# Optimization experiments

Hardware: AMD Instinct MI355X
Metric: run time of the kernel (lower is better)

## Reference

```python
import jax, jax.numpy as jnp
import numpy as np

A_BIT = 4
W_BIT = 4
IN_PLANES = 32
OUT_PLANES = 32
EXPANSION = 6
PLANES = EXPANSION * IN_PLANES  # 192


def _fake_quant(x, bits):
    """Per-tensor symmetric fake quantization to `bits` (round + clip, dequantized)."""
    qmax = 2.0 ** (bits - 1) - 1.0
    scale = jnp.maximum(jnp.max(jnp.abs(x)) / qmax, 1e-8)
    y = x / scale
    # straight-through round
    yq = jnp.clip(y + jax.lax.stop_gradient(jnp.round(y) - y), -qmax - 1.0, qmax)
    return yq * scale


def _conv(x, w, stride=1, padding=0, groups=1):
    return jax.lax.conv_general_dilated(
        x, w,
        window_strides=(stride, stride),
        padding=[(padding, padding), (padding, padding)],
        dimension_numbers=("NCHW", "OIHW", "NCHW"),
        feature_group_count=groups,
    )


def _qconv(x, w, stride=1, padding=0, groups=1):
    # FuseConv2dQ: fake-quantize activation (a_bit) and weight (w_bit), then fp conv
    return _conv(_fake_quant(x, A_BIT), _fake_quant(w, W_BIT),
                 stride=stride, padding=padding, groups=groups)


def setup_inputs() -> dict:
    key = jax.random.key(0)
    k0, k1, k2, k3 = jax.random.split(key, 4)
    x = jax.random.normal(k0, (32, IN_PLANES, 112, 112), dtype=jnp.float32)
    # conv1: 1x1 expand  [planes, in_planes, 1, 1]
    w1 = jax.random.normal(k1, (PLANES, IN_PLANES, 1, 1), dtype=jnp.float32) * 0.1
    # conv2: 3x3 depthwise, groups=planes -> [planes, 1, 3, 3]
    w2 = jax.random.normal(k2, (PLANES, 1, 3, 3), dtype=jnp.float32) * 0.1
    # conv3: 1x1 project  [out_planes, planes, 1, 1]
    w3 = jax.random.normal(k3, (OUT_PLANES, PLANES, 1, 1), dtype=jnp.float32) * 0.1
    return {"x": x, "w1": w1, "w2": w2, "w3": w3}


def reference(x, w1, w2, w3):
    out = jax.nn.relu(_qconv(x, w1))                                   # expand 1x1
    out = jax.nn.relu(_qconv(out, w2, stride=1, padding=1, groups=PLANES))  # depthwise 3x3
    out = _qconv(out, w3)                                              # project 1x1
    # stride == 1 and in_planes == out_planes -> identity shortcut
    return out + x
```

## Files before the change

### kernel.cpp

```cpp
#include <hip/hip_runtime.h>

#define NB   32
#define CIN  32
#define PL   192
#define CP   96
#define NG1  4
#define NG3  24
#define HH   112
#define WID  112
#define HW   12544
#define COUT 32
#define SEGS 784
#define SEGROW 7
#define PXB  1568
#define SEG8 14
#define RT8  784

#define W2POFF 64
#define W1NOFF (W2POFF + PL*4)
#define W3NOFF (W1NOFF + NG1*PL)
#define Q1OFF_BYTES 65536
#define QBYTES ((size_t)NB*CP*HW)

__device__ __forceinline__ int sdot4(unsigned int a, unsigned int b, int c) {
#if defined(__has_builtin) && __has_builtin(__builtin_amdgcn_sdot4)
  return __builtin_amdgcn_sdot4((int)a, (int)b, c, false);
#else
#pragma unroll
  for (int i = 0; i < 4; ++i)
    c += ((int)(a << (24 - 8 * i)) >> 24) * ((int)(b << (24 - 8 * i)) >> 24);
  return c;
#endif
}

__device__ __forceinline__ int sdot8(unsigned int a, unsigned int b, int c) {
#if defined(__has_builtin) && __has_builtin(__builtin_amdgcn_sdot8)
  return __builtin_amdgcn_sdot8((int)a, (int)b, c, false);
#else
#pragma unroll
  for (int i = 0; i < 8; ++i)
    c += ((int)(a << (28 - 4 * i)) >> 28) * ((int)(b << (28 - 4 * i)) >> 28);
  return c;
#endif
}

template <int SH>
__device__ __forceinline__ unsigned int winsh(unsigned int hi, unsigned int lo) {
#if defined(__has_builtin) && __has_builtin(__builtin_amdgcn_perm)
  const unsigned int sel = (SH == 1) ? 0x04030201u : (SH == 2) ? 0x05040302u : 0x06050403u;
  return __builtin_amdgcn_perm(hi, lo, sel);
#else
  return (lo >> (8 * SH)) | (hi << (32 - 8 * SH));
#endif
}

__device__ __forceinline__ float quant87(float v, float s) {
  return fminf(fmaxf(rintf(v / s), -8.0f), 7.0f);
}

__device__ __forceinline__ void block_max_commit(int lmax, int* __restrict__ slot) {
  __shared__ int red[4];
  for (int o = 32; o; o >>= 1) lmax = max(lmax, __shfl_down(lmax, o));
  if ((threadIdx.x & 63) == 0) red[threadIdx.x >> 6] = lmax;
  __syncthreads();
  if (threadIdx.x == 0) {
    int m = max(max(red[0], red[1]), max(red[2], red[3]));
    int cur = *(const volatile int*)slot;
    if (m > cur) atomicMax(slot, m);
  }
}

__global__ void kzero(int* __restrict__ wsi) {
  if (threadIdx.x < 16) wsi[threadIdx.x] = 0;
}

__global__ void kmax_x(const float* __restrict__ x, int n4, int* __restrict__ slot) {
  const float4* x4 = (const float4*)x;
  float m = 0.f;
  for (int i = blockIdx.x * blockDim.x + threadIdx.x; i < n4; i += gridDim.x * blockDim.x) {
    float4 v = x4[i];
    m = fmaxf(fmaxf(fabsf(v.x), fabsf(v.y)), fmaxf(fmaxf(fabsf(v.z), fabsf(v.w)), m));
  }
  block_max_commit(__float_as_int(m), slot);
}

__global__ void kmax_w(const float* __restrict__ w1, const float* __restrict__ w2,
                       const float* __restrict__ w3, int* __restrict__ slots) {
  const float* p; int n;
  if (blockIdx.x == 0)      { p = w1; n = PL * CIN; }
  else if (blockIdx.x == 1) { p = w2; n = PL * 9; }
  else                      { p = w3; n = COUT * PL; }
  float m = 0.f;
  for (int i = threadIdx.x; i < n; i += blockDim.x) m = fmaxf(m, fabsf(p[i]));
  for (int o = 32; o; o >>= 1) m = fmaxf(m, __shfl_down(m, o));
  if ((threadIdx.x & 63) == 0) atomicMax(slots + 1 + blockIdx.x, __float_as_int(m));
}

__global__ void kprep(const float* __restrict__ w1, const float* __restrict__ w2,
                      const float* __restrict__ w3, float* __restrict__ wsf) {
  int* wsi = (int*)wsf;
  unsigned int* wsu = (unsigned int*)wsf;
  __shared__ float ss[4];
  if (threadIdx.x == 0) {
    float sx  = fmaxf(__int_as_float(wsi[0]) / 7.0f, 1e-8f);
    float sw1 = fmaxf(__int_as_float(wsi[1]) / 7.0f, 1e-8f);
    float sw2 = fmaxf(__int_as_float(wsi[2]) / 7.0f, 1e-8f);
    float sw3 = fmaxf(__int_as_float(wsi[3]) / 7.0f, 1e-8f);
    wsf[8] = sx; wsf[9] = sw1; wsf[10] = sw2; wsf[11] = sw3;
    ss[1] = sw1; ss[2] = sw2; ss[3] = sw3;
  }
  __syncthreads();
  float sw1 = ss[1], sw2 = ss[2], sw3 = ss[3];
  for (int i = threadIdx.x; i < NG1 * PL; i += blockDim.x) {
    int g = i / PL, o = i - g * PL;
    unsigned int wrd = 0;
    for (int k = 0; k < 8; ++k)
      wrd |= ((unsigned)((int)quant87(w1[o * CIN + 8 * g + k], sw1) & 15)) << (4 * k);
    wsu[W1NOFF + i] = wrd;
  }
  for (int ch = threadIdx.x; ch < PL; ch += blockDim.x) {
    unsigned int r[3];
    for (int k = 0; k < 3; ++k) {
      int b0 = (int)quant87(w2[ch * 9 + 3 * k],     sw2) & 255;
      int b1 = (int)quant87(w2[ch * 9 + 3 * k + 1], sw2) & 255;
      int b2 = (int)quant87(w2[ch * 9 + 3 * k + 2], sw2) & 255;
      r[k] = (unsigned)(b0 | (b1 << 8) | (b2 << 16));
    }
    uint4 wv; wv.x = r[0]; wv.y = r[1]; wv.z = r[2]; wv.w = 0;
    *(uint4*)&wsu[W2POFF + ch * 4] = wv;
  }
  for (int i = threadIdx.x; i < NG3 * COUT; i += blockDim.x) {
    int g = i / COUT, o = i - g * COUT;
    unsigned int wrd = 0;
    for (int k = 0; k < 8; ++k)
      wrd |= ((unsigned)((int)quant87(w3[o * PL + 8 * g + k], sw3) & 15)) << (4 * k);
    wsu[W3NOFF + i] = wrd;
  }
}

__launch_bounds__(256)
__global__ void kquantx(const float* __restrict__ x, const float* __restrict__ wsf,
                        unsigned int* __restrict__ xq4) {
  float sx = wsf[8];
  int t = blockIdx.x * 256 + threadIdx.x;
  int s = t % SEGS;
  int g = (t / SEGS) & 3;
  int n = t / (SEGS * 4);
  const float* xb = x + ((size_t)n * CIN + 8 * g) * HW + s * 16;
  unsigned int* dst = xq4 + ((size_t)n * NG1 + g) * HW + s * 16;
#pragma unroll
  for (int c4 = 0; c4 < 4; ++c4) {
    unsigned int w[4] = {0u, 0u, 0u, 0u};
#pragma unroll
    for (int k = 0; k < 8; ++k) {
      float4 v = *(const float4*)(xb + (size_t)k * HW + c4 * 4);
      w[0] |= ((unsigned)((int)quant87(v.x, sx) & 15)) << (4 * k);
      w[1] |= ((unsigned)((int)quant87(v.y, sx) & 15)) << (4 * k);
      w[2] |= ((unsigned)((int)quant87(v.z, sx) & 15)) << (4 * k);
      w[3] |= ((unsigned)((int)quant87(v.w, sx) & 15)) << (4 * k);
    }
    uint4 o; o.x = w[0]; o.y = w[1]; o.z = w[2]; o.w = w[3];
    *(uint4*)(dst + c4 * 4) = o;
  }
}

template <int STORE>
__launch_bounds__(256)
__global__ void kconv1(const unsigned int* __restrict__ xq4, const float* __restrict__ wsf,
                       unsigned char* __restrict__ q1, int* __restrict__ maxslot) {
  __shared__ unsigned int lw[NG1 * 64];
  __shared__ unsigned char lut[2176];
  const int* wsi = (const int*)wsf;
  const unsigned int* wsu = (const unsigned int*)wsf;
  int ogb = blockIdx.x / PXB;
  int pxb = blockIdx.x - ogb * PXB;
  {
    int g = threadIdx.x >> 6, ol = threadIdx.x & 63;
    lw[threadIdx.x] = wsu[W1NOFF + g * PL + ogb * 64 + ol];
  }
  if (STORE) {
    float S1 = wsf[8] * wsf[9];
    float sh1 = fmaxf((S1 * (float)wsi[4]) / 7.0f, 1e-8f);
    for (int i = threadIdx.x; i < 2176; i += 256)
      lut[i] = (unsigned char)fminf(rintf((S1 * (float)i) / sh1), 7.0f);
  }
  __syncthreads();
  int og = threadIdx.x >> 5;
  int pxl = threadIdx.x & 31;
  int gp = pxb * 256 + pxl * 8;
  int n = gp / HW, pos = gp - n * HW;
  const unsigned int* xw = xq4 + (size_t)n * NG1 * HW + pos;
  int acc[8][8] = {};
#pragma unroll
  for (int g = 0; g < NG1; ++g) {
    uint4 xa = *(const uint4*)(xw + (size_t)g * HW);
    uint4 xb = *(const uint4*)(xw + (size_t)g * HW + 4);
    uint4 wa = *(const uint4*)&lw[g * 64 + og * 8];
    uint4 wb = *(const uint4*)&lw[g * 64 + og * 8 + 4];
    unsigned int xv[8] = {xa.x, xa.y, xa.z, xa.w, xb.x, xb.y, xb.z, xb.w};
    unsigned int wv[8] = {wa.x, wa.y, wa.z, wa.w, wb.x, wb.y, wb.z, wb.w};
#pragma unroll
    for (int o = 0; o < 8; ++o)
#pragma unroll
      for (int j = 0; j < 8; ++j)
        acc[o][j] = sdot8(xv[j], wv[o], acc[o][j]);
  }
  if (!STORE) {
    int lmax = 0;
#pragma unroll
    for (int o = 0; o < 8; ++o)
#pragma unroll
      for (int j = 0; j < 8; ++j)
        lmax = max(lmax, max(acc[o][j], 0));
    block_max_commit(lmax, maxslot);
  } else {
    int cpb = ogb * 32 + og * 4;
#pragma unroll
    for (int m = 0; m < 4; ++m) {
      unsigned int b0 = 0, b1 = 0;
#pragma unroll
      for (int j = 0; j < 4; ++j) {
        int i0 = max(acc[2 * m][j], 0);
        int i1 = max(acc[2 * m + 1][j], 0);
        b0 |= ((unsigned)(lut[i0] | (lut[i1] << 4))) << (8 * j);
        int i2 = max(acc[2 * m][4 + j], 0);
        int i3 = max(acc[2 * m + 1][4 + j], 0);
        b1 |= ((unsigned)(lut[i2] | (lut[i3] << 4))) << (8 * j);
      }
      uint2 w; w.x = b0; w.y = b1;
      *(uint2*)(q1 + ((size_t)n * CP + cpb + m) * HW + pos) = w;
    }
  }
}

template <int STORE>
__launch_bounds__(256)
__global__ void kconv2(const unsigned char* __restrict__ q1, const float* __restrict__ wsf,
                       unsigned int* __restrict__ q2w, int* __restrict__ maxslot) {
  const int* wsi = (const int*)wsf;
  const uint4* w2p = (const uint4*)((const unsigned int*)wsf + W2POFF);
  __shared__ unsigned char lut[512];
  if (STORE) {
    float S1 = wsf[8] * wsf[9];
    float sh1 = fmaxf((S1 * (float)wsi[4]) / 7.0f, 1e-8f);
    float S2 = sh1 * wsf[10];
    float sh2 = fmaxf((S2 * (float)wsi[5]) / 7.0f, 1e-8f);
    for (int i = threadIdx.x; i < 512; i += 256)
      lut[i] = (unsigned char)fminf(rintf((S2 * (float)i) / sh2), 7.0f);
    __syncthreads();
  }
  int gid = blockIdx.x * 256 + threadIdx.x;
  int nG = gid / RT8;
  int t  = gid - nG * RT8;
  int r2 = t / SEG8;
  int c  = t - r2 * SEG8;
  int y0 = r2 * 2, x0 = c * 8;
  int n = nG / NG3, G = nG - n * NG3;
  int cp0 = G * 4;
  const unsigned char* base = q1 + ((size_t)n * CP + cp0) * HW;
  const unsigned int M = 0x0F0F0F0Fu;
  unsigned int w0acc[8], w1acc[8];
  if (STORE) {
#pragma unroll
    for (int j = 0; j < 8; ++j) { w0acc[j] = 0u; w1acc[j] = 0u; }
  }
  int lmax = 0;
#pragma unroll
  for (int p = 0; p < 4; ++p) {
    int ch2 = (cp0 + p) * 2;
    uint4 wv0 = w2p[ch2];
    uint4 wv1 = w2p[ch2 + 1];
    unsigned int wr0[3] = {wv0.x, wv0.y, wv0.z};
    unsigned int wr1[3] = {wv1.x, wv1.y, wv1.z};
    int a0r0[8] = {}, a1r0[8] = {}, a0r1[8] = {}, a1r1[8] = {};
#pragma unroll
    for (int R = 0; R < 4; ++R) {
      unsigned int yy = (unsigned)(y0 - 1 + R);
      bool vld = yy < (unsigned)HH;
      const unsigned char* rp = base + (size_t)p * HW + (size_t)yy * WID + x0;
      uint2 u; u.x = u.y = 0u;
      unsigned int lwr = 0u, rwr = 0u;
      if (vld) u = *(const uint2*)rp;
      if (vld && c > 0) lwr = *(const unsigned int*)(rp - 4);
      if (vld && c < SEG8 - 1) rwr = *(const unsigned int*)(rp + 8);
      unsigned int SL[4], SHS[4];
      SL[0] = lwr & M;  SHS[0] = (lwr >> 4) & M;
      SL[1] = u.x & M;  SHS[1] = (u.x >> 4) & M;
      SL[2] = u.y & M;  SHS[2] = (u.y >> 4) & M;
      SL[3] = rwr & M;  SHS[3] = (rwr >> 4) & M;
#pragma unroll
      for (int j = 0; j < 8; ++j) {
        const int m = j >> 2, s = j & 3;
        unsigned int Wl, Wh;
        if (s == 1)      { Wl = SL[m + 1];                      Wh = SHS[m + 1]; }
        else if (s == 2) { Wl = winsh<1>(SL[m + 2], SL[m + 1]); Wh = winsh<1>(SHS[m + 2], SHS[m + 1]); }
        else if (s == 3) { Wl = winsh<2>(SL[m + 2], SL[m + 1]); Wh = winsh<2>(SHS[m + 2], SHS[m + 1]); }
        else             { Wl = winsh<3>(SL[m + 1], SL[m]);     Wh = winsh<3>(SHS[m + 1], SHS[m]); }
        if (R <= 2) {
          a0r0[j] = sdot4(Wl, wr0[R], a0r0[j]);
          a1r0[j] = sdot4(Wh, wr1[R], a1r0[j]);
        }
        if (R >= 1) {
          a0r1[j] = sdot4(Wl, wr0[R - 1], a0r1[j]);
          a1r1[j] = sdot4(Wh, wr1[R - 1], a1r1[j]);
        }
      }
    }
    if (!STORE) {
#pragma unroll
      for (int j = 0; j < 8; ++j) {
        lmax = max(lmax, max(a0r0[j], a1r0[j]));
        lmax = max(lmax, max(a0r1[j], a1r1[j]));
      }
    } else {
#pragma unroll
      for (int j = 0; j < 8; ++j) {
        unsigned int b0 = (unsigned)lut[max(a0r0[j], 0)] | ((unsigned)lut[max(a1r0[j], 0)] << 4);
        unsigned int b1 = (unsigned)lut[max(a0r1[j], 0)] | ((unsigned)lut[max(a1r1[j], 0)] << 4);
        w0acc[j] |= b0 << (8 * p);
        w1acc[j] |= b1 << (8 * p);
      }
    }
  }
  if (!STORE) {
    block_max_commit(max(lmax, 0), maxslot);
  } else {
    unsigned int* d0 = q2w + (size_t)nG * HW + (size_t)y0 * WID + x0;
    unsigned int* d1 = d0 + WID;
    uint4 o;
    o.x = w0acc[0]; o.y = w0acc[1]; o.z = w0acc[2]; o.w = w0acc[3];
    *(uint4*)d0 = o;
    o.x = w0acc[4]; o.y = w0acc[5]; o.z = w0acc[6]; o.w = w0acc[7];
    *(uint4*)(d0 + 4) = o;
    o.x = w1acc[0]; o.y = w1acc[1]; o.z = w1acc[2]; o.w = w1acc[3];
    *(uint4*)d1 = o;
    o.x = w1acc[4]; o.y = w1acc[5]; o.z = w1acc[6]; o.w = w1acc[7];
    *(uint4*)(d1 + 4) = o;
  }
}

__launch_bounds__(256)
__global__ void kconv3(const unsigned int* __restrict__ q2w, const float* __restrict__ x,
                       const float* __restrict__ wsf, float* __restrict__ out) {
  __shared__ unsigned int lw[NG3 * COUT];
  const unsigned int* wsu = (const unsigned int*)wsf;
  for (int i = threadIdx.x; i < NG3 * COUT; i += 256) lw[i] = wsu[W3NOFF + i];
  const int* wsi = (const int*)wsf;
  float S1 = wsf[8] * wsf[9];
  float sh1 = fmaxf((S1 * (float)wsi[4]) / 7.0f, 1e-8f);
  float S2 = sh1 * wsf[10];
  float sh2 = fmaxf((S2 * (float)wsi[5]) / 7.0f, 1e-8f);
  float S3 = sh2 * wsf[11];
  __syncthreads();
  int og = threadIdx.x >> 6;
  int lane = threadIdx.x & 63;
  int gp = blockIdx.x * 256 + lane * 4;
  int n = gp / HW, pos = gp - n * HW;
  const unsigned int* qp = q2w + (size_t)n * NG3 * HW + pos;
  int acc[8][4] = {};
#pragma unroll 4
  for (int g = 0; g < NG3; ++g) {
    uint4 qv = *(const uint4*)(qp + (size_t)g * HW);
    uint4 wa = *(const uint4*)&lw[g * COUT + og * 8];
    uint4 wb = *(const uint4*)&lw[g * COUT + og * 8 + 4];
    unsigned int pv[4] = {qv.x, qv.y, qv.z, qv.w};
    unsigned int wv[8] = {wa.x, wa.y, wa.z, wa.w, wb.x, wb.y, wb.z, wb.w};
#pragma unroll
    for (int o = 0; o < 8; ++o)
#pragma unroll
      for (int j = 0; j < 4; ++j)
        acc[o][j] = sdot8(pv[j], wv[o], acc[o][j]);
  }
  int ob = og * 8;
#pragma unroll
  for (int o = 0; o < 8; ++o) {
    const float* xp = x + ((size_t)n * COUT + ob + o) * HW + pos;
    float* op = out + ((size_t)n * COUT + ob + o) * HW + pos;
    float4 xv = *(const float4*)xp;
    float4 r;
    r.x = fmaf(S3, (float)acc[o][0], xv.x);
    r.y = fmaf(S3, (float)acc[o][1], xv.y);
    r.z = fmaf(S3, (float)acc[o][2], xv.z);
    r.w = fmaf(S3, (float)acc[o][3], xv.w);
    *(float4*)op = r;
  }
}

extern "C" void kernel_launch(void* const* d_in, const int* in_sizes, int n_in,
                              void* d_out, int out_size, void* d_ws, size_t ws_size,
                              hipStream_t stream) {
  const float* x  = (const float*)d_in[0];
  const float* w1 = (const float*)d_in[1];
  const float* w2 = (const float*)d_in[2];
  const float* w3 = (const float*)d_in[3];
  float* out = (float*)d_out;

  float* wsf = (float*)d_ws;
  int* wsi = (int*)d_ws;
  unsigned char* q1 = (unsigned char*)d_ws + Q1OFF_BYTES;
  unsigned int* q2w = (unsigned int*)(q1 + QBYTES);
  unsigned int* xq4 = (unsigned int*)d_out;

  kzero<<<1, 64, 0, stream>>>(wsi);

  int n4 = in_sizes[0] / 4;
  kmax_x<<<1024, 256, 0, stream>>>(x, n4, wsi + 0);
  kmax_w<<<3, 256, 0, stream>>>(w1, w2, w3, wsi);
  kprep<<<1, 256, 0, stream>>>(w1, w2, w3, wsf);
  kquantx<<<NB * NG1 * SEGS / 256, 256, 0, stream>>>(x, wsf, xq4);

  kconv1<0><<<3 * PXB, 256, 0, stream>>>(xq4, wsf, q1, wsi + 4);
  kconv1<1><<<3 * PXB, 256, 0, stream>>>(xq4, wsf, q1, wsi + 4);

  int nblk2 = NB * NG3 * RT8 / 256;
  kconv2<0><<<nblk2, 256, 0, stream>>>(q1, wsf, q2w, wsi + 5);
  kconv2<1><<<nblk2, 256, 0, stream>>>(q1, wsf, q2w, wsi + 5);

  kconv3<<<NB * HW / 256, 256, 0, stream>>>(q2w, x, wsf, out);
}
```

Measured before the change: 184.4 us.

## Stage depthwise conv input bands in LDS with one output row per thread

The depthwise 3x3 kernel now has each block stage a 16-row band (plus halo) of four packed channels into shared memory, then each thread computes one output row of 8 pixels from LDS. This replaces the per-thread global loads of four rows with halo words and the two-rows-per-thread register blocking. The goal is to cut redundant global reads and turn halo reuse into LDS reuse. In exchange, only 224 of 256 threads do work, every block pays a barrier, and per-thread ILP is lower.

```diff
diff --git a/kernel.cpp b/kernel.cpp
--- a/kernel.cpp
+++ b/kernel.cpp
@@ -11,10 +11,13 @@
 #define HW   12544
 #define COUT 32
 #define SEGS 784
-#define SEGROW 7
 #define PXB  1568
-#define SEG8 14
-#define RT8  784
+#define B2ROWS  16
+#define B2STAGE 18
+#define B2SEGS  14
+#define NBAND   7
+#define STG_DW  2016
+#define PLROW_DW 504
 
 #define W2POFF 64
 #define W1NOFF (W2POFF + PL*4)
@@ -237,9 +240,18 @@
 __launch_bounds__(256)
 __global__ void kconv2(const unsigned char* __restrict__ q1, const float* __restrict__ wsf,
                        unsigned int* __restrict__ q2w, int* __restrict__ maxslot) {
+  __shared__ unsigned int ltile[4 + STG_DW + 4];
+  __shared__ unsigned char lut[512];
   const int* wsi = (const int*)wsf;
   const uint4* w2p = (const uint4*)((const unsigned int*)wsf + W2POFF);
-  __shared__ unsigned char lut[512];
+
+  int bi = blockIdx.x;
+  int b  = bi % NBAND;
+  int nG = bi / NBAND;
+  int n = nG / NG3, G = nG - n * NG3;
+  int cp0 = G * 4;
+  int ystart = b * B2ROWS - 1;
+
   if (STORE) {
     float S1 = wsf[8] * wsf[9];
     float sh1 = fmaxf((S1 * (float)wsi[4]) / 7.0f, 1e-8f);
@@ -247,95 +259,93 @@
     float sh2 = fmaxf((S2 * (float)wsi[5]) / 7.0f, 1e-8f);
     for (int i = threadIdx.x; i < 512; i += 256)
       lut[i] = (unsigned char)fminf(rintf((S2 * (float)i) / sh2), 7.0f);
-    __syncthreads();
-  }
-  int gid = blockIdx.x * 256 + threadIdx.x;
-  int nG = gid / RT8;
-  int t  = gid - nG * RT8;
-  int r2 = t / SEG8;
-  int c  = t - r2 * SEG8;
-  int y0 = r2 * 2, x0 = c * 8;
-  int n = nG / NG3, G = nG - n * NG3;
-  int cp0 = G * 4;
-  const unsigned char* base = q1 + ((size_t)n * CP + cp0) * HW;
+  }
+  {
+    const unsigned int* q1w = (const unsigned int*)(q1 + ((size_t)n * CP + cp0) * HW);
+#pragma unroll
+    for (int k = 0; k < 8; ++k) {
+      int idx = threadIdx.x + k * 256;
+      if (idx < STG_DW) {
+        int p   = idx / PLROW_DW;
+        int rem = idx - p * PLROW_DW;
+        int rho = rem / 28;
+        int xd  = rem - rho * 28;
+        int y = ystart + rho;
+        unsigned int v = 0u;
+        if ((unsigned)y < (unsigned)HH)
+          v = q1w[(size_t)p * (HW / 4) + y * 28 + xd];
+        ltile[4 + idx] = v;
+      }
+    }
+  }
+  __syncthreads();
+
+  int tid = threadIdx.x;
+  bool active = tid < B2SEGS * B2ROWS;
+  int r = tid / B2SEGS;
+  int s = tid - r * B2SEGS;
+  int x0 = s * 8;
+  const char* lbase = (const char*)ltile + 16;
   const unsigned int M = 0x0F0F0F0Fu;
-  unsigned int w0acc[8], w1acc[8];
-  if (STORE) {
-#pragma unroll
-    for (int j = 0; j < 8; ++j) { w0acc[j] = 0u; w1acc[j] = 0u; }
-  }
+  unsigned int wacc[8];
+#pragma unroll
+  for (int j = 0; j < 8; ++j) wacc[j] = 0u;
   int lmax = 0;
-#pragma unroll
-  for (int p = 0; p < 4; ++p) {
-    int ch2 = (cp0 + p) * 2;
-    uint4 wv0 = w2p[ch2];
-    uint4 wv1 = w2p[ch2 + 1];
-    unsigned int wr0[3] = {wv0.x, wv0.y, wv0.z};
-    unsigned int wr1[3] = {wv1.x, wv1.y, wv1.z};
-    int a0r0[8] = {}, a1r0[8] = {}, a0r1[8] = {}, a1r1[8] = {};
-#pragma unroll
-    for (int R = 0; R < 4; ++R) {
-      unsigned int yy = (unsigned)(y0 - 1 + R);
-      bool vld = yy < (unsigned)HH;
-      const unsigned char* rp = base + (size_t)p * HW + (size_t)yy * WID + x0;
-      uint2 u; u.x = u.y = 0u;
-      unsigned int lwr = 0u, rwr = 0u;
-      if (vld) u = *(const uint2*)rp;
-      if (vld && c > 0) lwr = *(const unsigned int*)(rp - 4);
-      if (vld && c < SEG8 - 1) rwr = *(const unsigned int*)(rp + 8);
-      unsigned int SL[4], SHS[4];
-      SL[0] = lwr & M;  SHS[0] = (lwr >> 4) & M;
-      SL[1] = u.x & M;  SHS[1] = (u.x >> 4) & M;
-      SL[2] = u.y & M;  SHS[2] = (u.y >> 4) & M;
-      SL[3] = rwr & M;  SHS[3] = (rwr >> 4) & M;
-#pragma unroll
-      for (int j = 0; j < 8; ++j) {
-        const int m = j >> 2, s = j & 3;
-        unsigned int Wl, Wh;
-        if (s == 1)      { Wl = SL[m + 1];                      Wh = SHS[m + 1]; }
-        else if (s == 2) { Wl = winsh<1>(SL[m + 2], SL[m + 1]); Wh = winsh<1>(SHS[m + 2], SHS[m + 1]); }
-        else if (s == 3) { Wl = winsh<2>(SL[m + 2], SL[m + 1]); Wh = winsh<2>(SHS[m + 2], SHS[m + 1]); }
-        else             { Wl = winsh<3>(SL[m + 1], SL[m]);     Wh = winsh<3>(SHS[m + 1], SHS[m]); }
-        if (R <= 2) {
-          a0r0[j] = sdot4(Wl, wr0[R], a0r0[j]);
-          a1r0[j] = sdot4(Wh, wr1[R], a1r0[j]);
+  if (active) {
+#pragma unroll
+    for (int p = 0; p < 4; ++p) {
+      int ch2 = (cp0 + p) * 2;
+      uint4 wv0 = w2p[ch2];
+      uint4 wv1 = w2p[ch2 + 1];
+      unsigned int wr0[3] = {wv0.x, wv0.y, wv0.z};
+      unsigned int wr1[3] = {wv1.x, wv1.y, wv1.z};
+      int a0[8] = {}, a1[8] = {};
+#pragma unroll
+      for (int R = 0; R < 3; ++R) {
+        const char* rowp = lbase + (p * B2STAGE + r + R) * 112 + x0;
+        uint2 u = *(const uint2*)rowp;
+        unsigned int lwr = (s == 0) ? 0u : *(const unsigned int*)(rowp - 4);
+        unsigned int rwr = (s == B2SEGS - 1) ? 0u : *(const unsigned int*)(rowp + 8);
+        unsigned int SL[4], SH[4];
+        SL[0] = lwr & M;  SH[0] = (lwr >> 4) & M;
+        SL[1] = u.x & M;  SH[1] = (u.x >> 4) & M;
+        SL[2] = u.y & M;  SH[2] = (u.y >> 4) & M;
+        SL[3] = rwr & M;  SH[3] = (rwr >> 4) & M;
+#pragma unroll
+        for (int j = 0; j < 8; ++j) {
+          const int m = j >> 2, sh = j & 3;
+          unsigned int Wl, Wh;
+          if (sh == 1)      { Wl = SL[m + 1];                      Wh = SH[m + 1]; }
+          else if (sh == 2) { Wl = winsh<1>(SL[m + 2], SL[m + 1]); Wh = winsh<1>(SH[m + 2], SH[m + 1]); }
+          else if (sh == 3) { Wl = winsh<2>(SL[m + 2], SL[m + 1]); Wh = winsh<2>(SH[m + 2], SH[m + 1]); }
+          else              { Wl = winsh<3>(SL[m + 1], SL[m]);     Wh = winsh<3>(SH[m + 1], SH[m]); }
+          a0[j] = sdot4(Wl, wr0[R], a0[j]);
+          a1[j] = sdot4(Wh, wr1[R], a1[j]);
         }
-        if (R >= 1) {
-          a0r1[j] = sdot4(Wl, wr0[R - 1], a0r1[j]);
-          a1r1[j] = sdot4(Wh, wr1[R - 1], a1r1[j]);
+      }
+      if (!STORE) {
+#pragma unroll
+        for (int j = 0; j < 8; ++j)
+          lmax = max(lmax, max(a0[j], a1[j]));
+      } else {
+#pragma unroll
+        for (int j = 0; j < 8; ++j) {
+          unsigned int by = (unsigned)lut[max(a0[j], 0)] | ((unsigned)lut[max(a1[j], 0)] << 4);
+          wacc[j] |= by << (8 * p);
         }
       }
     }
-    if (!STORE) {
-#pragma unroll
-      for (int j = 0; j < 8; ++j) {
-        lmax = max(lmax, max(a0r0[j], a1r0[j]));
-        lmax = max(lmax, max(a0r1[j], a1r1[j]));
-      }
-    } else {
-#pragma unroll
-      for (int j = 0; j < 8; ++j) {
-        unsigned int b0 = (unsigned)lut[max(a0r0[j], 0)] | ((unsigned)lut[max(a1r0[j], 0)] << 4);
-        unsigned int b1 = (unsigned)lut[max(a0r1[j], 0)] | ((unsigned)lut[max(a1r1[j], 0)] << 4);
-        w0acc[j] |= b0 << (8 * p);
-        w1acc[j] |= b1 << (8 * p);
-      }
-    }
   }
   if (!STORE) {
     block_max_commit(max(lmax, 0), maxslot);
-  } else {
-    unsigned int* d0 = q2w + (size_t)nG * HW + (size_t)y0 * WID + x0;
-    unsigned int* d1 = d0 + WID;
+  } else if (active) {
+    int y = b * B2ROWS + r;
+    unsigned int* d0 = q2w + (size_t)nG * HW + (size_t)y * WID + x0;
     uint4 o;
-    o.x = w0acc[0]; o.y = w0acc[1]; o.z = w0acc[2]; o.w = w0acc[3];
+    o.x = wacc[0]; o.y = wacc[1]; o.z = wacc[2]; o.w = wacc[3];
     *(uint4*)d0 = o;
-    o.x = w0acc[4]; o.y = w0acc[5]; o.z = w0acc[6]; o.w = w0acc[7];
+    o.x = wacc[4]; o.y = wacc[5]; o.z = wacc[6]; o.w = wacc[7];
     *(uint4*)(d0 + 4) = o;
-    o.x = w1acc[0]; o.y = w1acc[1]; o.z = w1acc[2]; o.w = w1acc[3];
-    *(uint4*)d1 = o;
-    o.x = w1acc[4]; o.y = w1acc[5]; o.z = w1acc[6]; o.w = w1acc[7];
-    *(uint4*)(d1 + 4) = o;
   }
 }
 
@@ -412,7 +422,7 @@
   kconv1<0><<<3 * PXB, 256, 0, stream>>>(xq4, wsf, q1, wsi + 4);
   kconv1<1><<<3 * PXB, 256, 0, stream>>>(xq4, wsf, q1, wsi + 4);
 
-  int nblk2 = NB * NG3 * RT8 / 256;
+  int nblk2 = NB * NG3 * NBAND;
   kconv2<0><<<nblk2, 256, 0, stream>>>(q1, wsf, q2w, wsi + 5);
   kconv2<1><<<nblk2, 256, 0, stream>>>(q1, wsf, q2w, wsi + 5);
 
```

After: 204.7 us. +11.0%, slower.

## Use nibble-packed sdot8 for depthwise conv and merge max-reduction kernels

Applied to the files above, without the earlier changes.

The depthwise 3x3 conv switches from sdot4 on unpacked low/high nibble lanes to sdot8 on packed 4-bit bytes. The weights are repacked so that one channel sits in the low nibbles and the other in the high nibbles, which removes the nibble masking and shift work per row. Row loads become unconditional with clamped offsets and select-based masking, and a signed LUT of 1024 entries absorbs the ReLU clamp. The x-max and weight-max kernels are merged into one launch. Correctness depends on the cross-nibble products in sdot8 landing only on the intended weight nibbles, which the zeroed weight nibbles are meant to guarantee.

```diff
diff --git a/kernel.cpp b/kernel.cpp
--- a/kernel.cpp
+++ b/kernel.cpp
@@ -11,27 +11,15 @@
 #define HW   12544
 #define COUT 32
 #define SEGS 784
-#define SEGROW 7
 #define PXB  1568
 #define SEG8 14
 #define RT8  784
 
-#define W2POFF 64
-#define W1NOFF (W2POFF + PL*4)
+#define W2NOFF 64
+#define W1NOFF (W2NOFF + CP*8)
 #define W3NOFF (W1NOFF + NG1*PL)
 #define Q1OFF_BYTES 65536
 #define QBYTES ((size_t)NB*CP*HW)
-
-__device__ __forceinline__ int sdot4(unsigned int a, unsigned int b, int c) {
-#if defined(__has_builtin) && __has_builtin(__builtin_amdgcn_sdot4)
-  return __builtin_amdgcn_sdot4((int)a, (int)b, c, false);
-#else
-#pragma unroll
-  for (int i = 0; i < 4; ++i)
-    c += ((int)(a << (24 - 8 * i)) >> 24) * ((int)(b << (24 - 8 * i)) >> 24);
-  return c;
-#endif
-}
 
 __device__ __forceinline__ int sdot8(unsigned int a, unsigned int b, int c) {
 #if defined(__has_builtin) && __has_builtin(__builtin_amdgcn_sdot8)
@@ -74,26 +62,28 @@
   if (threadIdx.x < 16) wsi[threadIdx.x] = 0;
 }
 
-__global__ void kmax_x(const float* __restrict__ x, int n4, int* __restrict__ slot) {
-  const float4* x4 = (const float4*)x;
+__global__ void kmax_all(const float* __restrict__ x, int n4,
+                         const float* __restrict__ w1, const float* __restrict__ w2,
+                         const float* __restrict__ w3, int* __restrict__ wsi) {
   float m = 0.f;
-  for (int i = blockIdx.x * blockDim.x + threadIdx.x; i < n4; i += gridDim.x * blockDim.x) {
-    float4 v = x4[i];
-    m = fmaxf(fmaxf(fabsf(v.x), fabsf(v.y)), fmaxf(fmaxf(fabsf(v.z), fabsf(v.w)), m));
-  }
-  block_max_commit(__float_as_int(m), slot);
-}
-
-__global__ void kmax_w(const float* __restrict__ w1, const float* __restrict__ w2,
-                       const float* __restrict__ w3, int* __restrict__ slots) {
-  const float* p; int n;
-  if (blockIdx.x == 0)      { p = w1; n = PL * CIN; }
-  else if (blockIdx.x == 1) { p = w2; n = PL * 9; }
-  else                      { p = w3; n = COUT * PL; }
-  float m = 0.f;
-  for (int i = threadIdx.x; i < n; i += blockDim.x) m = fmaxf(m, fabsf(p[i]));
-  for (int o = 32; o; o >>= 1) m = fmaxf(m, __shfl_down(m, o));
-  if ((threadIdx.x & 63) == 0) atomicMax(slots + 1 + blockIdx.x, __float_as_int(m));
+  int slot;
+  if (blockIdx.x < 1024) {
+    const float4* x4 = (const float4*)x;
+    for (int i = blockIdx.x * blockDim.x + threadIdx.x; i < n4; i += 1024 * blockDim.x) {
+      float4 v = x4[i];
+      m = fmaxf(fmaxf(fabsf(v.x), fabsf(v.y)), fmaxf(fmaxf(fabsf(v.z), fabsf(v.w)), m));
+    }
+    slot = 0;
+  } else {
+    const float* p; int n;
+    int w = blockIdx.x - 1024;
+    if (w == 0)      { p = w1; n = PL * CIN; }
+    else if (w == 1) { p = w2; n = PL * 9; }
+    else             { p = w3; n = COUT * PL; }
+    for (int i = threadIdx.x; i < n; i += blockDim.x) m = fmaxf(m, fabsf(p[i]));
+    slot = 1 + w;
+  }
+  block_max_commit(__float_as_int(m), wsi + slot);
 }
 
 __global__ void kprep(const float* __restrict__ w1, const float* __restrict__ w2,
@@ -118,16 +108,21 @@
       wrd |= ((unsigned)((int)quant87(w1[o * CIN + 8 * g + k], sw1) & 15)) << (4 * k);
     wsu[W1NOFF + i] = wrd;
   }
-  for (int ch = threadIdx.x; ch < PL; ch += blockDim.x) {
-    unsigned int r[3];
-    for (int k = 0; k < 3; ++k) {
-      int b0 = (int)quant87(w2[ch * 9 + 3 * k],     sw2) & 255;
-      int b1 = (int)quant87(w2[ch * 9 + 3 * k + 1], sw2) & 255;
-      int b2 = (int)quant87(w2[ch * 9 + 3 * k + 2], sw2) & 255;
-      r[k] = (unsigned)(b0 | (b1 << 8) | (b2 << 16));
-    }
-    uint4 wv; wv.x = r[0]; wv.y = r[1]; wv.z = r[2]; wv.w = 0;
-    *(uint4*)&wsu[W2POFF + ch * 4] = wv;
+  for (int cp = threadIdx.x; cp < CP; cp += blockDim.x) {
+    unsigned int d[8];
+    for (int R = 0; R < 3; ++R) {
+      int a0 = (int)quant87(w2[(2 * cp) * 9 + 3 * R],     sw2) & 15;
+      int a1 = (int)quant87(w2[(2 * cp) * 9 + 3 * R + 1], sw2) & 15;
+      int a2 = (int)quant87(w2[(2 * cp) * 9 + 3 * R + 2], sw2) & 15;
+      int b0 = (int)quant87(w2[(2 * cp + 1) * 9 + 3 * R],     sw2) & 15;
+      int b1 = (int)quant87(w2[(2 * cp + 1) * 9 + 3 * R + 1], sw2) & 15;
+      int b2 = (int)quant87(w2[(2 * cp + 1) * 9 + 3 * R + 2], sw2) & 15;
+      d[2 * R]     = (unsigned)(a0 | (a1 << 8) | (a2 << 16));
+      d[2 * R + 1] = (unsigned)((b0 << 4) | (b1 << 12) | (b2 << 20));
+    }
+    d[6] = 0u; d[7] = 0u;
+    unsigned int* dst = wsu + W2NOFF + cp * 8;
+    for (int k = 0; k < 8; ++k) dst[k] = d[k];
   }
   for (int i = threadIdx.x; i < NG3 * COUT; i += blockDim.x) {
     int g = i / COUT, o = i - g * COUT;
@@ -238,15 +233,18 @@
 __global__ void kconv2(const unsigned char* __restrict__ q1, const float* __restrict__ wsf,
                        unsigned int* __restrict__ q2w, int* __restrict__ maxslot) {
   const int* wsi = (const int*)wsf;
-  const uint4* w2p = (const uint4*)((const unsigned int*)wsf + W2POFF);
-  __shared__ unsigned char lut[512];
+  const unsigned int* w2n = (const unsigned int*)wsf + W2NOFF;
+  __shared__ unsigned char lut[1024];
   if (STORE) {
     float S1 = wsf[8] * wsf[9];
     float sh1 = fmaxf((S1 * (float)wsi[4]) / 7.0f, 1e-8f);
     float S2 = sh1 * wsf[10];
     float sh2 = fmaxf((S2 * (float)wsi[5]) / 7.0f, 1e-8f);
-    for (int i = threadIdx.x; i < 512; i += 256)
-      lut[i] = (unsigned char)fminf(rintf((S2 * (float)i) / sh2), 7.0f);
+    for (int i = threadIdx.x; i < 1024; i += 256) {
+      int a = i - 512;
+      lut[i] = (a <= 0) ? (unsigned char)0
+                        : (unsigned char)fminf(rintf((S2 * (float)a) / sh2), 7.0f);
+    }
     __syncthreads();
   }
   int gid = blockIdx.x * 256 + threadIdx.x;
@@ -257,52 +255,64 @@
   int y0 = r2 * 2, x0 = c * 8;
   int n = nG / NG3, G = nG - n * NG3;
   int cp0 = G * 4;
-  const unsigned char* base = q1 + ((size_t)n * CP + cp0) * HW;
-  const unsigned int M = 0x0F0F0F0Fu;
-  unsigned int w0acc[8], w1acc[8];
+  const unsigned char* base = q1 + ((size_t)n * CP + cp0) * HW + x0;
+  int rofs[4]; bool rok[4];
+#pragma unroll
+  for (int R = 0; R < 4; ++R) {
+    int yy = y0 - 1 + R;
+    rok[R] = (unsigned)yy < (unsigned)HH;
+    rofs[R] = min(max(yy, 0), HH - 1) * WID;
+  }
+  bool has_l = (c > 0), has_r = (c < SEG8 - 1);
+  unsigned int wacc[16];
   if (STORE) {
 #pragma unroll
-    for (int j = 0; j < 8; ++j) { w0acc[j] = 0u; w1acc[j] = 0u; }
+    for (int j = 0; j < 16; ++j) wacc[j] = 0u;
   }
   int lmax = 0;
 #pragma unroll
   for (int p = 0; p < 4; ++p) {
-    int ch2 = (cp0 + p) * 2;
-    uint4 wv0 = w2p[ch2];
-    uint4 wv1 = w2p[ch2 + 1];
-    unsigned int wr0[3] = {wv0.x, wv0.y, wv0.z};
-    unsigned int wr1[3] = {wv1.x, wv1.y, wv1.z};
+    unsigned int wc0[3], wc1[3];
+    {
+      const unsigned int* wp = w2n + (size_t)(cp0 + p) * 8;
+      uint4 wa = *(const uint4*)wp;
+      uint2 wb = *(const uint2*)(wp + 4);
+      wc0[0] = wa.x; wc1[0] = wa.y; wc0[1] = wa.z; wc1[1] = wa.w;
+      wc0[2] = wb.x; wc1[2] = wb.y;
+    }
+    const unsigned char* pb = base + (size_t)p * HW;
     int a0r0[8] = {}, a1r0[8] = {}, a0r1[8] = {}, a1r1[8] = {};
 #pragma unroll
     for (int R = 0; R < 4; ++R) {
-      unsigned int yy = (unsigned)(y0 - 1 + R);
-      bool vld = yy < (unsigned)HH;
-      const unsigned char* rp = base + (size_t)p * HW + (size_t)yy * WID + x0;
-      uint2 u; u.x = u.y = 0u;
-      unsigned int lwr = 0u, rwr = 0u;
-      if (vld) u = *(const uint2*)rp;
-      if (vld && c > 0) lwr = *(const unsigned int*)(rp - 4);
-      if (vld && c < SEG8 - 1) rwr = *(const unsigned int*)(rp + 8);
-      unsigned int SL[4], SHS[4];
-      SL[0] = lwr & M;  SHS[0] = (lwr >> 4) & M;
-      SL[1] = u.x & M;  SHS[1] = (u.x >> 4) & M;
-      SL[2] = u.y & M;  SHS[2] = (u.y >> 4) & M;
-      SL[3] = rwr & M;  SHS[3] = (rwr >> 4) & M;
-#pragma unroll
-      for (int j = 0; j < 8; ++j) {
-        const int m = j >> 2, s = j & 3;
-        unsigned int Wl, Wh;
-        if (s == 1)      { Wl = SL[m + 1];                      Wh = SHS[m + 1]; }
-        else if (s == 2) { Wl = winsh<1>(SL[m + 2], SL[m + 1]); Wh = winsh<1>(SHS[m + 2], SHS[m + 1]); }
-        else if (s == 3) { Wl = winsh<2>(SL[m + 2], SL[m + 1]); Wh = winsh<2>(SHS[m + 2], SHS[m + 1]); }
-        else             { Wl = winsh<3>(SL[m + 1], SL[m]);     Wh = winsh<3>(SHS[m + 1], SHS[m]); }
-        if (R <= 2) {
-          a0r0[j] = sdot4(Wl, wr0[R], a0r0[j]);
-          a1r0[j] = sdot4(Wh, wr1[R], a1r0[j]);
+      const unsigned char* rp = pb + rofs[R];
+      uint2 u = *(const uint2*)rp;
+      unsigned int lwr = *(const unsigned int*)(rp - 4);
+      unsigned int rwr = *(const unsigned int*)(rp + 8);
+      u.x = rok[R] ? u.x : 0u;
+      u.y = rok[R] ? u.y : 0u;
+      lwr = (rok[R] && has_l) ? lwr : 0u;
+      rwr = (rok[R] && has_r) ? rwr : 0u;
+      unsigned int W[8];
+      W[0] = winsh<3>(u.x, lwr);
+      W[1] = u.x;
+      W[2] = winsh<1>(u.y, u.x);
+      W[3] = winsh<2>(u.y, u.x);
+      W[4] = winsh<3>(u.y, u.x);
+      W[5] = u.y;
+      W[6] = winsh<1>(rwr, u.y);
+      W[7] = winsh<2>(rwr, u.y);
+      if (R <= 2) {
+#pragma unroll
+        for (int j = 0; j < 8; ++j) {
+          a0r0[j] = sdot8(W[j], wc0[R], a0r0[j]);
+          a1r0[j] = sdot8(W[j], wc1[R], a1r0[j]);
         }
-        if (R >= 1) {
-          a0r1[j] = sdot4(Wl, wr0[R - 1], a0r1[j]);
-          a1r1[j] = sdot4(Wh, wr1[R - 1], a1r1[j]);
+      }
+      if (R >= 1) {
+#pragma unroll
+        for (int j = 0; j < 8; ++j) {
+          a0r1[j] = sdot8(W[j], wc0[R - 1], a0r1[j]);
+          a1r1[j] = sdot8(W[j], wc1[R - 1], a1r1[j]);
         }
       }
     }
@@ -315,10 +325,10 @@
     } else {
 #pragma unroll
       for (int j = 0; j < 8; ++j) {
-        unsigned int b0 = (unsigned)lut[max(a0r0[j], 0)] | ((unsigned)lut[max(a1r0[j], 0)] << 4);
-        unsigned int b1 = (unsigned)lut[max(a0r1[j], 0)] | ((unsigned)lut[max(a1r1[j], 0)] << 4);
-        w0acc[j] |= b0 << (8 * p);
-        w1acc[j] |= b1 << (8 * p);
+        unsigned int b0 = (unsigned)lut[512 + a0r0[j]] | ((unsigned)lut[512 + a1r0[j]] << 4);
+        unsigned int b1 = (unsigned)lut[512 + a0r1[j]] | ((unsigned)lut[512 + a1r1[j]] << 4);
+        wacc[j]     |= b0 << (8 * p);
+        wacc[8 + j] |= b1 << (8 * p);
       }
     }
   }
@@ -328,13 +338,13 @@
     unsigned int* d0 = q2w + (size_t)nG * HW + (size_t)y0 * WID + x0;
     unsigned int* d1 = d0 + WID;
     uint4 o;
-    o.x = w0acc[0]; o.y = w0acc[1]; o.z = w0acc[2]; o.w = w0acc[3];
+    o.x = wacc[0]; o.y = wacc[1]; o.z = wacc[2]; o.w = wacc[3];
     *(uint4*)d0 = o;
-    o.x = w0acc[4]; o.y = w0acc[5]; o.z = w0acc[6]; o.w = w0acc[7];
+    o.x = wacc[4]; o.y = wacc[5]; o.z = wacc[6]; o.w = wacc[7];
     *(uint4*)(d0 + 4) = o;
-    o.x = w1acc[0]; o.y = w1acc[1]; o.z = w1acc[2]; o.w = w1acc[3];
+    o.x = wacc[8]; o.y = wacc[9]; o.z = wacc[10]; o.w = wacc[11];
     *(uint4*)d1 = o;
-    o.x = w1acc[4]; o.y = w1acc[5]; o.z = w1acc[6]; o.w = w1acc[7];
+    o.x = wacc[12]; o.y = wacc[13]; o.z = wacc[14]; o.w = wacc[15];
     *(uint4*)(d1 + 4) = o;
   }
 }
@@ -404,8 +414,7 @@
   kzero<<<1, 64, 0, stream>>>(wsi);
 
   int n4 = in_sizes[0] / 4;
-  kmax_x<<<1024, 256, 0, stream>>>(x, n4, wsi + 0);
-  kmax_w<<<3, 256, 0, stream>>>(w1, w2, w3, wsi);
+  kmax_all<<<1027, 256, 0, stream>>>(x, n4, w1, w2, w3, wsi);
   kprep<<<1, 256, 0, stream>>>(w1, w2, w3, wsf);
   kquantx<<<NB * NG1 * SEGS / 256, 256, 0, stream>>>(x, wsf, xq4);
 
```

Result: faster. 160.8 us (-12.8%).
